# Performance work log

Measured on AMD Instinct MI355X. Metric: run time of the kernel, lower is better.

The kernel has to match this reference:

```python
import jax, jax.numpy as jnp
import numpy as np

N, L = 5, 2097152
WIDTH = 11  # max_pool1d kernel width in the original


def setup_inputs() -> dict:
    key = jax.random.key(0)
    k1, k2 = jax.random.split(key)
    rppg = jax.random.normal(k1, (N, L), dtype=jnp.float32)
    ppg = jax.random.normal(k2, (N, L), dtype=jnp.float32)
    return {"rppg": rppg, "ppg": ppg, "fs": 30, "epoch": 15}


def _normalize(x):
    # normalize_torch: per-signal standardization
    mu = x.mean(axis=1, keepdims=True)
    sd = x.std(axis=1, keepdims=True)
    return (x - mu) / sd


def _window_max(x, width):
    # sliding max over centered window of `width`, same padding (-inf pad)
    return jax.lax.reduce_window(x, -jnp.inf, jax.lax.max,
                                 (1, width), (1, 1),
                                 [(0, 0), (width // 2, width // 2)])


def _mean_hr(x, fs):
    # A position p is a 'nice peak' iff max_pool argmax at p equals p,
    # i.e. x[p] is the max of its own centered window (ties have measure 0
    # for continuous signals). unique()+masking collapses to this mask.
    w = _window_max(x, WIDTH)
    m1 = x == w                                            # [N, L] peak mask
    npk = m1.sum(axis=1, keepdims=True).astype(x.dtype)
    mean_pk = (x * m1).sum(axis=1, keepdims=True) / npk    # mean of peak values
    m = m1 & (x > mean_pk / 2)                             # amplitude-filtered peaks
    idx = jnp.arange(x.shape[1])
    vals = jnp.where(m, idx, -1)
    # previous peak index strictly before p (fixed-shape replacement for diff
    # over a variable-length peak index list)
    prev = jnp.pad(jax.lax.cummax(vals, axis=1)[:, :-1], ((0, 0), (1, 0)),
                   constant_values=-1)
    valid = m & (prev >= 0)                                # one entry per inter-peak gap
    gaps = (idx[None, :] - prev).astype(x.dtype)
    inv = jnp.where(valid, 1.0 / gaps, 0.0)
    # mean(60 / (gap / fs)) = 60 * fs * mean(1 / gap)
    return (60.0 * fs) * inv.sum(axis=1) / valid.sum(axis=1).astype(x.dtype)


def reference(rppg, ppg, fs, epoch):
    ppg = _normalize(ppg.reshape(N, -1))
    rppg = _normalize(rppg.reshape(N, -1))
    ppg_hr = _mean_hr(ppg, fs)
    rppg_hr = _mean_hr(rppg, fs)
    # hr_score = mean_i |ppg_hr - rppg_hr| / ppg_hr  (peak_score is computed
    # in the original but not returned)
    return jnp.mean(jnp.abs(ppg_hr - rppg_hr) / ppg_hr)
```

## Files before the change

kernel.cpp:

```cpp
#include <hip/hip_runtime.h>
#include <math.h>

namespace {

constexpr int LNUM = 2097152;
constexpr int NROW = 5;
constexpr int NSER = 10;
constexpr int TPB = 256;
constexpr int CHUNK = 4096;
constexpr int CPR = LNUM / CHUNK;
constexpr int NBLK = NSER * CPR;
constexpr int KIT = 4;

struct Agg { int first; int last; int c; double s; };

__device__ __forceinline__ Agg combine(const Agg& a, const Agg& b) {
  Agg r;
  r.first = (a.first >= 0) ? a.first : b.first;
  r.last  = (b.last >= 0) ? b.last : a.last;
  r.s = a.s + b.s;
  r.c = a.c + b.c;
  if (a.last >= 0 && b.first >= 0) {
    r.s += 1.0 / (double)(b.first - a.last);
    r.c += 1;
  }
  return r;
}

__device__ __forceinline__ const float* row_ptr(const float* rppg,
                                                const float* ppg, int rw) {
  return (rw < NROW) ? rppg + (size_t)rw * LNUM
                     : ppg + (size_t)(rw - NROW) * LNUM;
}

__device__ __forceinline__ void window4(const float* __restrict__ x, int p0,
                                        float X[4], float w[4]) {
  const float4 f = *reinterpret_cast<const float4*>(x + p0);
  X[0] = f.x; X[1] = f.y; X[2] = f.z; X[3] = f.w;
  float Y[14];
  Y[5] = X[0]; Y[6] = X[1]; Y[7] = X[2]; Y[8] = X[3];
  Y[1] = __shfl_up(X[0], 1);  Y[2] = __shfl_up(X[1], 1);
  Y[3] = __shfl_up(X[2], 1);  Y[4] = __shfl_up(X[3], 1);
  Y[0] = __shfl_up(X[3], 2);
  Y[9] = __shfl_down(X[0], 1);  Y[10] = __shfl_down(X[1], 1);
  Y[11] = __shfl_down(X[2], 1); Y[12] = __shfl_down(X[3], 1);
  Y[13] = __shfl_down(X[0], 2);
  const int lane = threadIdx.x & 63;
  if (lane == 0) {
#pragma unroll
    for (int j = 0; j < 5; ++j) {
      int g = p0 - 5 + j;
      Y[j] = (g >= 0) ? x[g] : -INFINITY;
    }
  } else if (lane == 1) {
    int g = p0 - 5;
    Y[0] = (g >= 0) ? x[g] : -INFINITY;
  }
  if (lane == 63) {
#pragma unroll
    for (int j = 0; j < 5; ++j) {
      int g = p0 + 4 + j;
      Y[9 + j] = (g < LNUM) ? x[g] : -INFINITY;
    }
  } else if (lane == 62) {
    int g = p0 + 8;
    Y[13] = (g < LNUM) ? x[g] : -INFINITY;
  }
  float m2[13];
#pragma unroll
  for (int i = 0; i < 13; ++i) m2[i] = fmaxf(Y[i], Y[i + 1]);
  float m4[11];
#pragma unroll
  for (int i = 0; i < 11; ++i) m4[i] = fmaxf(m2[i], m2[i + 2]);
  float m8[7];
#pragma unroll
  for (int i = 0; i < 7; ++i) m8[i] = fmaxf(m4[i], m4[i + 4]);
#pragma unroll
  for (int t = 0; t < 4; ++t) w[t] = fmaxf(m8[t], m8[t + 3]);
}

__global__ __launch_bounds__(TPB) void stats_kernel(
    const float* __restrict__ rppg, const float* __restrict__ ppg,
    double* __restrict__ psum, double* __restrict__ ppk,
    int* __restrict__ pnpk) {
  const int bid = blockIdx.x;
  const int rw = bid >> 9;
  const int chunk = bid & (CPR - 1);
  const float* x = row_ptr(rppg, ppg, rw);
  const int lane = threadIdx.x & 63;
  const int wid = threadIdx.x >> 6;
  const int segbase = chunk * CHUNK + wid * 1024;

  double tsum = 0.0, tpk = 0.0;
  int tn = 0;
  for (int k = 0; k < KIT; ++k) {
    const int p0 = segbase + k * 256 + 4 * lane;
    float X[4], w[4];
    window4(x, p0, X, w);
#pragma unroll
    for (int t = 0; t < 4; ++t) {
      tsum += (double)X[t];
      if (X[t] == w[t]) { tpk += (double)X[t]; ++tn; }
    }
  }
#pragma unroll
  for (int off = 32; off > 0; off >>= 1) {
    tsum += __shfl_down(tsum, off);
    tpk  += __shfl_down(tpk, off);
    tn   += __shfl_down(tn, off);
  }
  __shared__ double wsum[4], wpk[4];
  __shared__ int wn[4];
  if (lane == 0) { wsum[wid] = tsum; wpk[wid] = tpk; wn[wid] = tn; }
  __syncthreads();
  if (threadIdx.x == 0) {
    psum[bid] = wsum[0] + wsum[1] + wsum[2] + wsum[3];
    ppk[bid]  = wpk[0] + wpk[1] + wpk[2] + wpk[3];
    pnpk[bid] = wn[0] + wn[1] + wn[2] + wn[3];
  }
}

__global__ __launch_bounds__(TPB) void thresh_kernel(
    const double* __restrict__ psum, const double* __restrict__ ppk,
    const int* __restrict__ pnpk, double* __restrict__ thr) {
  const int r = blockIdx.x;
  const int t = threadIdx.x;
  const int lane = t & 63;
  const int wid = t >> 6;
  double s0 = psum[r * CPR + t] + psum[r * CPR + t + 256];
  double p0 = ppk[r * CPR + t] + ppk[r * CPR + t + 256];
  int n0 = pnpk[r * CPR + t] + pnpk[r * CPR + t + 256];
#pragma unroll
  for (int off = 32; off > 0; off >>= 1) {
    s0 += __shfl_down(s0, off);
    p0 += __shfl_down(p0, off);
    n0 += __shfl_down(n0, off);
  }
  __shared__ double ws[4], wp[4];
  __shared__ int wn[4];
  if (lane == 0) { ws[wid] = s0; wp[wid] = p0; wn[wid] = n0; }
  __syncthreads();
  if (t == 0) {
    double S = ws[0] + ws[1] + ws[2] + ws[3];
    double P = wp[0] + wp[1] + wp[2] + wp[3];
    double Nn = (double)(wn[0] + wn[1] + wn[2] + wn[3]);
    thr[r] = 0.5 * (S / (double)LNUM + P / Nn);
  }
}

__global__ __launch_bounds__(TPB) void gap_kernel(
    const float* __restrict__ rppg, const float* __restrict__ ppg,
    const double* __restrict__ thr,
    int* __restrict__ cfirst, int* __restrict__ clast,
    double* __restrict__ csum, int* __restrict__ ccnt) {
  const int bid = blockIdx.x;
  const int rw = bid >> 9;
  const int chunk = bid & (CPR - 1);
  const float* x = row_ptr(rppg, ppg, rw);
  const float th = (float)thr[rw];
  const int lane = threadIdx.x & 63;
  const int wid = threadIdx.x >> 6;
  const int segbase = chunk * CHUNK + wid * 1024;

  Agg wacc; wacc.first = -1; wacc.last = -1; wacc.c = 0; wacc.s = 0.0;
  for (int k = 0; k < KIT; ++k) {
    const int p0 = segbase + k * 256 + 4 * lane;
    float X[4], w[4];
    window4(x, p0, X, w);
    Agg a; a.first = -1; a.last = -1; a.c = 0; a.s = 0.0;
#pragma unroll
    for (int t = 0; t < 4; ++t) {
      if (X[t] == w[t] && X[t] > th) {
        int p = p0 + t;
        if (a.last >= 0) { a.s += 1.0 / (double)(p - a.last); ++a.c; }
        else a.first = p;
        a.last = p;
      }
    }
#pragma unroll
    for (int off = 1; off < 64; off <<= 1) {
      Agg b;
      b.first = __shfl_down(a.first, off);
      b.last  = __shfl_down(a.last, off);
      b.c     = __shfl_down(a.c, off);
      b.s     = __shfl_down(a.s, off);
      a = combine(a, b);
    }
    Agg t0;
    t0.first = __shfl(a.first, 0);
    t0.last  = __shfl(a.last, 0);
    t0.c     = __shfl(a.c, 0);
    t0.s     = __shfl(a.s, 0);
    wacc = combine(wacc, t0);
  }

  __shared__ Agg waggs[4];
  if (lane == 0) waggs[wid] = wacc;
  __syncthreads();
  if (threadIdx.x == 0) {
    Agg r = waggs[0];
    r = combine(r, waggs[1]);
    r = combine(r, waggs[2]);
    r = combine(r, waggs[3]);
    cfirst[bid] = r.first; clast[bid] = r.last;
    csum[bid] = r.s; ccnt[bid] = r.c;
  }
}

__global__ __launch_bounds__(TPB) void final_kernel(
    const int* __restrict__ cfirst, const int* __restrict__ clast,
    const double* __restrict__ csum, const int* __restrict__ ccnt,
    const int* __restrict__ fsp, float* __restrict__ out) {
  __shared__ Agg waggs[4];
  __shared__ double shr[NSER];
  const int t = threadIdx.x;
  const int lane = t & 63;
  const int wid = t >> 6;
  for (int r = 0; r < NSER; ++r) {
    const int i0 = r * CPR + 2 * t;
    Agg a0; a0.first = cfirst[i0];     a0.last = clast[i0];
    a0.c = ccnt[i0];                   a0.s = csum[i0];
    Agg a1; a1.first = cfirst[i0 + 1]; a1.last = clast[i0 + 1];
    a1.c = ccnt[i0 + 1];               a1.s = csum[i0 + 1];
    a0 = combine(a0, a1);
#pragma unroll
    for (int off = 1; off < 64; off <<= 1) {
      Agg b;
      b.first = __shfl_down(a0.first, off);
      b.last  = __shfl_down(a0.last, off);
      b.c     = __shfl_down(a0.c, off);
      b.s     = __shfl_down(a0.s, off);
      a0 = combine(a0, b);
    }
    if (lane == 0) waggs[wid] = a0;
    __syncthreads();
    if (t == 0) {
      Agg rr = waggs[0];
      rr = combine(rr, waggs[1]);
      rr = combine(rr, waggs[2]);
      rr = combine(rr, waggs[3]);
      shr[r] = 60.0 * (double)fsp[0] * rr.s / (double)rr.c;
    }
    __syncthreads();
  }
  if (t == 0) {
    double acc = 0.0;
    for (int r = 0; r < NROW; ++r)
      acc += fabs(shr[NROW + r] - shr[r]) / shr[NROW + r];
    out[0] = (float)(acc / (double)NROW);
  }
}

}

extern "C" void kernel_launch(void* const* d_in, const int* in_sizes, int n_in,
                              void* d_out, int out_size, void* d_ws, size_t ws_size,
                              hipStream_t stream) {
  const float* rppg = (const float*)d_in[0];
  const float* ppg  = (const float*)d_in[1];
  const int* fsp    = (const int*)d_in[2];
  float* out        = (float*)d_out;
  char* ws          = (char*)d_ws;

  double* psum   = (double*)(ws);
  double* ppk    = (double*)(ws + 40960);
  int*    pnpk   = (int*)(ws + 81920);
  double* csum   = (double*)(ws + 102400);
  int*    cfirst = (int*)(ws + 143360);
  int*    clast  = (int*)(ws + 163840);
  int*    ccnt   = (int*)(ws + 184320);
  double* thr    = (double*)(ws + 204800);

  stats_kernel<<<NBLK, TPB, 0, stream>>>(rppg, ppg, psum, ppk, pnpk);
  thresh_kernel<<<NSER, TPB, 0, stream>>>(psum, ppk, pnpk, thr);
  gap_kernel<<<NBLK, TPB, 0, stream>>>(rppg, ppg, thr, cfirst, clast, csum, ccnt);
  final_kernel<<<1, TPB, 0, stream>>>(cfirst, clast, csum, ccnt, fsp, out);
  (void)in_sizes; (void)n_in; (void)out_size; (void)ws_size;
}
```

Measured before the change: 185.6 us.

## Replace per-iteration aggregate shuffle reduction with max-scan prefix for previous peak

The gap kernel no longer reduces a full first/last/count/sum aggregate across the wavefront, with fp64 divisions, on every iteration. Each lane now keeps at most one peak per 4-element group, which is safe because the 11-wide window keeps peaks at least 6 apart. An integer max-scan with a carry across iterations finds each peak's predecessor, and sum, count and first are reduced only once at the end. This is meant to cut the heavy shuffle traffic and double-precision division cost. The reciprocal of the gap is now computed in float, which adds a small precision change.

```diff
diff --git a/kernel.cpp b/kernel.cpp
--- a/kernel.cpp
+++ b/kernel.cpp
@@ -1,5 +1,6 @@
 #include <hip/hip_runtime.h>
 #include <math.h>
+#include <limits.h>
 
 namespace {
 
@@ -162,40 +163,48 @@
   const int wid = threadIdx.x >> 6;
   const int segbase = chunk * CHUNK + wid * 1024;
 
-  Agg wacc; wacc.first = -1; wacc.last = -1; wacc.c = 0; wacc.s = 0.0;
+  double lsum = 0.0;
+  int lcnt = 0;
+  int lfirst = INT_MAX;
+  int carry = -1;
   for (int k = 0; k < KIT; ++k) {
     const int p0 = segbase + k * 256 + 4 * lane;
     float X[4], w[4];
     window4(x, p0, X, w);
-    Agg a; a.first = -1; a.last = -1; a.c = 0; a.s = 0.0;
-#pragma unroll
-    for (int t = 0; t < 4; ++t) {
-      if (X[t] == w[t] && X[t] > th) {
-        int p = p0 + t;
-        if (a.last >= 0) { a.s += 1.0 / (double)(p - a.last); ++a.c; }
-        else a.first = p;
-        a.last = p;
-      }
-    }
+    int pk = -1;
+#pragma unroll
+    for (int t = 0; t < 4; ++t)
+      if (X[t] == w[t] && X[t] > th) pk = p0 + t;
+    if (pk >= 0 && lfirst == INT_MAX) lfirst = pk;
+    int m = pk;
 #pragma unroll
     for (int off = 1; off < 64; off <<= 1) {
-      Agg b;
-      b.first = __shfl_down(a.first, off);
-      b.last  = __shfl_down(a.last, off);
-      b.c     = __shfl_down(a.c, off);
-      b.s     = __shfl_down(a.s, off);
-      a = combine(a, b);
-    }
-    Agg t0;
-    t0.first = __shfl(a.first, 0);
-    t0.last  = __shfl(a.last, 0);
-    t0.c     = __shfl(a.c, 0);
-    t0.s     = __shfl(a.s, 0);
-    wacc = combine(wacc, t0);
-  }
-
+      int u = __shfl_up(m, off);
+      if (lane >= off) m = max(m, u);
+    }
+    int excl = __shfl_up(m, 1);
+    int prev = (lane == 0) ? carry : max(excl, carry);
+    if (pk >= 0 && prev >= 0) {
+      lsum += (double)(1.0f / (float)(pk - prev));
+      ++lcnt;
+    }
+    int lastall = __shfl(m, 63);
+    carry = max(carry, lastall);
+  }
+#pragma unroll
+  for (int off = 32; off > 0; off >>= 1) {
+    lsum += __shfl_down(lsum, off);
+    lcnt += __shfl_down(lcnt, off);
+    lfirst = min(lfirst, __shfl_down(lfirst, off));
+  }
   __shared__ Agg waggs[4];
-  if (lane == 0) waggs[wid] = wacc;
+  if (lane == 0) {
+    Agg a;
+    a.first = (lfirst == INT_MAX) ? -1 : lfirst;
+    a.last = carry;
+    a.c = lcnt; a.s = lsum;
+    waggs[wid] = a;
+  }
   __syncthreads();
   if (threadIdx.x == 0) {
     Agg r = waggs[0];
```

Result: faster. 170.7 us (-8.0%).
